# Kernel tuning notes

Measured on AMD Instinct MI355X. Metric: run time of the kernel, lower is better.

The kernel has to match this reference:

```python
import jax, jax.numpy as jnp
import numpy as np

D_MODEL = 1024
NUM_HEADS = 16
D_K = D_MODEL // NUM_HEADS
THETA = 10000.0
BATCH, SEQ = 2, 2048


def apply_rope(x, token_positions, theta):
    # x: [..., heads, seq, d_k]; interleaved pair rotation
    d = x.shape[-1]
    inv_freq = theta ** (-jnp.arange(0, d, 2, dtype=jnp.float32) / d)  # [d/2]
    ang = token_positions.astype(jnp.float32)[:, None] * inv_freq[None, :]  # [seq, d/2]
    cos, sin = jnp.cos(ang), jnp.sin(ang)  # broadcast over batch/heads
    x_even = x[..., 0::2]
    x_odd = x[..., 1::2]
    out_even = x_even * cos - x_odd * sin
    out_odd = x_even * sin + x_odd * cos
    out = jnp.stack([out_even, out_odd], axis=-1)  # [..., seq, d/2, 2]
    return out.reshape(x.shape)


def setup_inputs() -> dict:
    key = jax.random.key(0)
    ks = jax.random.split(key, 5)
    scale = 1.0 / np.sqrt(D_MODEL)
    return {
        "x": jax.random.normal(ks[0], (BATCH, SEQ, D_MODEL), dtype=jnp.float32),
        "wq": jax.random.normal(ks[1], (D_MODEL, D_MODEL), dtype=jnp.float32) * scale,
        "wk": jax.random.normal(ks[2], (D_MODEL, D_MODEL), dtype=jnp.float32) * scale,
        "wv": jax.random.normal(ks[3], (D_MODEL, D_MODEL), dtype=jnp.float32) * scale,
        "wo": jax.random.normal(ks[4], (D_MODEL, D_MODEL), dtype=jnp.float32) * scale,
        "token_positions": jnp.arange(SEQ, dtype=jnp.int32),
    }


def reference(x, wq, wk, wv, wo, token_positions):
    B, S, _ = x.shape
    # fused-style QKV projections: weight layout is [d_out, d_in]
    xq = jnp.einsum("bsd,kd->bsk", x, wq)
    xk = jnp.einsum("bsd,kd->bsk", x, wk)
    xv = jnp.einsum("bsd,vd->bsv", x, wv)
    # split heads: [b, h, s, d_h]
    def split(t):
        return t.reshape(B, S, NUM_HEADS, D_K).transpose(0, 2, 1, 3)
    xq, xk, xv = split(xq), split(xk), split(xv)
    xq = apply_rope(xq, token_positions, THETA)
    xk = apply_rope(xk, token_positions, THETA)
    scores = jnp.einsum("bhqd,bhkd->bhqk", xq, xk) / jnp.sqrt(jnp.float32(D_K))
    causal = jnp.tril(jnp.ones((S, S), dtype=bool))
    scores = jnp.where(causal, scores, -jnp.inf)
    attn = jax.nn.softmax(scores, axis=-1)
    out = jnp.einsum("bhqk,bhkd->bhqd", attn, xv)
    out = out.transpose(0, 2, 1, 3).reshape(B, S, D_MODEL)  # merge heads
    return jnp.einsum("bsv,dv->bsd", out, wo)
```

## Files before the change

### kernel.cpp

```cpp
#include <hip/hip_runtime.h>

typedef __attribute__((ext_vector_type(8))) short short8;
typedef __attribute__((ext_vector_type(4))) short short4v;
typedef __attribute__((ext_vector_type(4))) float floatx4;

__device__ inline float b2f(ushort u) {
    union { uint i; float f; } c; c.i = ((uint)u) << 16; return c.f;
}
__device__ inline ushort f2b(float f) {
    union { uint i; float f; } c; c.f = f;
    uint i = c.i;
    uint r = (i + 0x7FFFu + ((i >> 16) & 1u)) >> 16;
    return (ushort)r;
}
__device__ inline ushort f2b_fast(float f) {
    union { uint i; float f; } c; c.f = f;
    return (ushort)((c.i + 0x8000u) >> 16);
}

__device__ __forceinline__ void load_lds16(const ushort* g, ushort* l) {
    __builtin_amdgcn_global_load_lds((const __attribute__((address_space(1))) void*)g,
                                     (__attribute__((address_space(3))) void*)l, 16, 0, 0);
}

__global__ __launch_bounds__(256) void rope_tab_k(const int* __restrict__ pos,
                                                  float2* __restrict__ tab) {
    const int idx = blockIdx.x * 256 + threadIdx.x;
    const int s = idx >> 5, fi = idx & 31;
    const float inv = exp2f(-(float)fi * 0.41524101186092557f);
    const float ang = (float)pos[s] * inv;
    float sn, cs;
    sincosf(ang, &sn, &cs);
    tab[idx] = make_float2(cs, sn);
}

__global__ __launch_bounds__(256) void cvt4_k(const float* __restrict__ x,
                                              const float* __restrict__ wq,
                                              const float* __restrict__ wk,
                                              const float* __restrict__ wv,
                                              ushort* __restrict__ xb,
                                              ushort* __restrict__ wqb,
                                              ushort* __restrict__ wkb,
                                              ushort* __restrict__ wvb) {
    const int blk = blockIdx.x;
    const float* in; ushort* out; int base;
    if (blk < 2048)      { in = x;  out = xb;  base = blk; }
    else if (blk < 2560) { in = wq; out = wqb; base = blk - 2048; }
    else if (blk < 3072) { in = wk; out = wkb; base = blk - 2560; }
    else                 { in = wv; out = wvb; base = blk - 3072; }
    const int i = (base * 256 + threadIdx.x) * 8;
    float4 f0 = *(const float4*)(in + i);
    float4 f1 = *(const float4*)(in + i + 4);
    ushort u[8] = {f2b(f0.x), f2b(f0.y), f2b(f0.z), f2b(f0.w),
                   f2b(f1.x), f2b(f1.y), f2b(f1.z), f2b(f1.w)};
    *(uint4*)(out + i) = *(const uint4*)u;
}

__global__ __launch_bounds__(256) void cvt_k(const float* __restrict__ in,
                                             ushort* __restrict__ out, int n) {
    const int i = (blockIdx.x * 256 + threadIdx.x) * 8;
    if (i >= n) return;
    float4 f0 = *(const float4*)(in + i);
    float4 f1 = *(const float4*)(in + i + 4);
    ushort u[8] = {f2b(f0.x), f2b(f0.y), f2b(f0.z), f2b(f0.w),
                   f2b(f1.x), f2b(f1.y), f2b(f1.z), f2b(f1.w)};
    *(uint4*)(out + i) = *(const uint4*)u;
}

template <bool OUTF32>
__device__ __forceinline__ void gemm_body(ushort* As, ushort* Bs,
                                          const ushort* __restrict__ A,
                                          const ushort* __restrict__ B,
                                          void* __restrict__ C,
                                          int N, int m0, int n0,
                                          bool doRope, const float2* __restrict__ tab) {
    const int tid = threadIdx.x;
    const int wave = tid >> 6, lane = tid & 63;
    const int quad = lane >> 4, l16 = lane & 15;
    const int wm = (wave >> 1) * 64, wn = (wave & 1) * 64;

    floatx4 acc[4][4] = {};

    const int cA = tid, cB = tid + 256;
    const int rA = cA >> 2, jgA = ((cA & 3) - (rA >> 1)) & 3;
    const int rB = cB >> 2, jgB = ((cB & 3) - (rB >> 1)) & 3;
    const ushort* gaA = A + (size_t)(m0 + rA) * 1024 + jgA * 8;
    const ushort* gaB = A + (size_t)(m0 + rB) * 1024 + jgB * 8;
    const ushort* gbA = B + (size_t)(n0 + rA) * 1024 + jgA * 8;
    const ushort* gbB = B + (size_t)(n0 + rB) * 1024 + jgB * 8;

    load_lds16(gaA, As + cA * 8);
    load_lds16(gaB, As + cB * 8);
    load_lds16(gbA, Bs + cA * 8);
    load_lds16(gbB, Bs + cB * 8);
    __syncthreads();

    for (int kt = 0; kt < 32; ++kt) {
        const int cur = kt & 1;
        if (kt + 1 < 32) {
            const int nb = (cur ^ 1) * 4096;
            load_lds16(gaA + (kt + 1) * 32, As + nb + cA * 8);
            load_lds16(gaB + (kt + 1) * 32, As + nb + cB * 8);
            load_lds16(gbA + (kt + 1) * 32, Bs + nb + cA * 8);
            load_lds16(gbB + (kt + 1) * 32, Bs + nb + cB * 8);
        }
        const ushort* as = As + cur * 4096;
        const ushort* bs = Bs + cur * 4096;
        short8 af[4], bf[4];
#pragma unroll
        for (int i = 0; i < 4; ++i) {
            const int ra = wm + i * 16 + l16;
            const int rb = wn + i * 16 + l16;
            af[i] = *(const short8*)(as + ra * 32 + (((quad + (ra >> 1)) & 3) << 3));
            bf[i] = *(const short8*)(bs + rb * 32 + (((quad + (rb >> 1)) & 3) << 3));
        }
#pragma unroll
        for (int mi = 0; mi < 4; ++mi)
#pragma unroll
            for (int ni = 0; ni < 4; ++ni)
                acc[mi][ni] = __builtin_amdgcn_mfma_f32_16x16x32_bf16(af[mi], bf[ni], acc[mi][ni], 0, 0, 0);
        __syncthreads();
    }
#pragma unroll
    for (int mi = 0; mi < 4; ++mi) {
        const int row = m0 + wm + mi * 16 + quad * 4;
#pragma unroll
        for (int ni = 0; ni < 4; ++ni) {
            const int col = n0 + wn + ni * 16 + l16;
            const int fi = ((wn + ni * 16 + l16) & 63) >> 1;
#pragma unroll
            for (int r = 0; r < 4; ++r) {
                float v = acc[mi][ni][r];
                if (doRope) {
                    const float other = __shfl_xor(v, 1);
                    const float2 cs = tab[((row + r) & 2047) * 32 + fi];
                    v = (col & 1) ? (other * cs.y + v * cs.x) : (v * cs.x - other * cs.y);
                }
                if (OUTF32) ((float*)C)[(size_t)(row + r) * N + col] = v;
                else        ((ushort*)C)[(size_t)(row + r) * N + col] = f2b(v);
            }
        }
    }
}

__global__ __launch_bounds__(256) void gemm_qkv(const ushort* __restrict__ xb,
                                                const ushort* __restrict__ wqb,
                                                const ushort* __restrict__ wkb,
                                                const ushort* __restrict__ wvb,
                                                ushort* __restrict__ q,
                                                ushort* __restrict__ k,
                                                ushort* __restrict__ vt,
                                                const float2* __restrict__ tab) {
    __shared__ __align__(16) ushort As[8192], Bs[8192];
    const int blk = blockIdx.x;
    const int job = blk >> 8, r = blk & 255;
    const ushort *A, *B;
    ushort* C;
    int N, m0, n0;
    bool rope;
    if (job == 0)      { A = xb;  B = wqb; C = q;  N = 1024; m0 = (r >> 3) * 128; n0 = (r & 7) * 128; rope = true; }
    else if (job == 1) { A = xb;  B = wkb; C = k;  N = 1024; m0 = (r >> 3) * 128; n0 = (r & 7) * 128; rope = true; }
    else               { A = wvb; B = xb;  C = vt; N = 4096; m0 = (r & 7) * 128;  n0 = (r >> 3) * 128; rope = false; }
    gemm_body<false>(As, Bs, A, B, C, N, m0, n0, rope, tab);
}

__global__ __launch_bounds__(256) void gemm_o(const ushort* __restrict__ A,
                                              const ushort* __restrict__ B,
                                              float* __restrict__ C) {
    __shared__ __align__(16) ushort As[8192], Bs[8192];
    gemm_body<true>(As, Bs, A, B, C, 1024, blockIdx.y * 128, blockIdx.x * 128, false, nullptr);
}

__global__ __launch_bounds__(256) void attn_k(const ushort* __restrict__ Qg,
                                              const ushort* __restrict__ Kg,
                                              const ushort* __restrict__ Vtg,
                                              ushort* __restrict__ Og) {
    __shared__ __align__(16) ushort Ks[2][4096];
    __shared__ __align__(16) ushort Vs[2][4096];

    const int tid = threadIdx.x;
    const int wave = tid >> 6, lane = tid & 63;
    const int quad = lane >> 4, l16 = lane & 15;
    const int blk = blockIdx.x;
    const int bh = blk & 31, pr = blk >> 5;
    const int b = bh >> 4, h = bh & 15;
    const int bq = b * 2048;
    const int wl = wave * 16 + l16;

    const int cA = tid, cB = tid + 256;
    const int sA = cA >> 3, jA = ((cA & 7) - sA) & 7;
    const int sB = cB >> 3, jB = ((cB & 7) - sB) & 7;
    const ushort* kgA = Kg + (size_t)(bq + sA) * 1024 + h * 64 + jA * 8;
    const ushort* kgB = Kg + (size_t)(bq + sB) * 1024 + h * 64 + jB * 8;
    const ushort* vgA = Vtg + (size_t)(h * 64 + sA) * 4096 + bq + jA * 8;
    const ushort* vgB = Vtg + (size_t)(h * 64 + sB) * 4096 + bq + jB * 8;

    const float SCL = 0.18033688011112042f;

    for (int half = 0; half < 2; ++half) {
        const int qt = half ? (31 - pr) : pr;
        const int nk = qt + 1;
        const int dt = nk - 1;

        const ushort* qrow = Qg + (size_t)(bq + qt * 64 + wl) * 1024 + h * 64 + quad * 8;
        const short8 qf0 = *(const short8*)qrow;
        const short8 qf1 = *(const short8*)(qrow + 32);

        floatx4 od[4] = {};
        float l_st = 0.0f;

        load_lds16(kgA, &Ks[0][cA * 8]);
        load_lds16(kgB, &Ks[0][cB * 8]);
        load_lds16(vgA, &Vs[0][cA * 8]);
        load_lds16(vgB, &Vs[0][cB * 8]);
        __syncthreads();

        for (int kt = 0; kt < nk; ++kt) {
            const int cur = kt & 1;
            if (kt + 1 < nk) {
                const int nxt = cur ^ 1;
                load_lds16(kgA + (size_t)(kt + 1) * 65536, &Ks[nxt][cA * 8]);
                load_lds16(kgB + (size_t)(kt + 1) * 65536, &Ks[nxt][cB * 8]);
                load_lds16(vgA + (kt + 1) * 64, &Vs[nxt][cA * 8]);
                load_lds16(vgB + (kt + 1) * 64, &Vs[nxt][cB * 8]);
            }
            const ushort* kb = Ks[cur];
            const ushort* vb = Vs[cur];

            floatx4 st[4];
#pragma unroll
            for (int cb = 0; cb < 4; ++cb) {
                const int s = cb * 16 + l16;
                const int ch0 = s * 8 + ((quad + s) & 7);
                const int ch1 = s * 8 + ((quad + 4 + s) & 7);
                short8 kf0 = *(const short8*)(kb + ch0 * 8);
                short8 kf1 = *(const short8*)(kb + ch1 * 8);
                floatx4 z = {};
                z = __builtin_amdgcn_mfma_f32_16x16x32_bf16(kf0, qf0, z, 0, 0, 0);
                z = __builtin_amdgcn_mfma_f32_16x16x32_bf16(kf1, qf1, z, 0, 0, 0);
                st[cb] = z;
            }

            const bool diag = (kt == dt);
            float pv[4][4];
            float sum = 0.0f;
#pragma unroll
            for (int cb = 0; cb < 4; ++cb) {
                const int scb = cb * 16 + quad * 4;
#pragma unroll
                for (int r = 0; r < 4; ++r) {
                    float e = exp2f(st[cb][r] * SCL);
                    if (diag && (scb + r > wl)) e = 0.0f;
                    pv[cb][r] = e;
                    sum += e;
                }
            }
            sum += __shfl_xor(sum, 16);
            sum += __shfl_xor(sum, 32);
            l_st += sum;

            short4v pb[4];
#pragma unroll
            for (int cb = 0; cb < 4; ++cb) {
                short4v pk;
#pragma unroll
                for (int r = 0; r < 4; ++r) pk[r] = (short)f2b_fast(pv[cb][r]);
                pb[cb] = pk;
            }
#pragma unroll
            for (int db = 0; db < 4; ++db) {
                const int d = db * 16 + l16;
#pragma unroll
                for (int cb = 0; cb < 4; ++cb) {
                    const int j = cb * 2 + (quad >> 1);
                    const int ch = d * 8 + ((j + d) & 7);
                    short4v vf = *(const short4v*)(vb + ch * 8 + (quad & 1) * 4);
                    od[db] = __builtin_amdgcn_mfma_f32_16x16x16bf16_1k(vf, pb[cb], od[db], 0, 0, 0);
                }
            }
            __syncthreads();
        }

        const float linv = 1.0f / l_st;
        ushort* orow = Og + (size_t)(bq + qt * 64 + wl) * 1024 + h * 64 + quad * 4;
#pragma unroll
        for (int db = 0; db < 4; ++db) {
            uint2 w;
            w.x = (uint)f2b(od[db][0] * linv) | ((uint)f2b(od[db][1] * linv) << 16);
            w.y = (uint)f2b(od[db][2] * linv) | ((uint)f2b(od[db][3] * linv) << 16);
            *(uint2*)(orow + db * 16) = w;
        }
    }
}

extern "C" void kernel_launch(void* const* d_in, const int* in_sizes, int n_in,
                              void* d_out, int out_size, void* d_ws, size_t ws_size,
                              hipStream_t stream) {
    const float* x  = (const float*)d_in[0];
    const float* wq = (const float*)d_in[1];
    const float* wk = (const float*)d_in[2];
    const float* wv = (const float*)d_in[3];
    const float* wo = (const float*)d_in[4];
    const int* pos  = (const int*)d_in[5];

    const size_t NX = (size_t)4096 * 1024;
    const size_t NW = (size_t)1024 * 1024;

    ushort* q_ws  = (ushort*)d_ws;
    ushort* k_ws  = q_ws + NX;
    ushort* vt_ws = k_ws + NX;
    ushort* o_ws  = vt_ws + NX;
    ushort* xb  = (ushort*)d_out;
    ushort* wqb = xb + NX;
    ushort* wkb = wqb + NW;
    ushort* wvb = wkb + NW;
    float2* tab = (float2*)(wvb + NW);

    rope_tab_k<<<dim3(256), 256, 0, stream>>>(pos, tab);
    cvt4_k<<<dim3(3584), 256, 0, stream>>>(x, wq, wk, wv, xb, wqb, wkb, wvb);
    gemm_qkv<<<dim3(768), 256, 0, stream>>>(xb, wqb, wkb, wvb, q_ws, k_ws, vt_ws, tab);
    attn_k<<<dim3(512), 256, 0, stream>>>(q_ws, k_ws, vt_ws, o_ws);
    cvt_k<<<dim3(512), 256, 0, stream>>>(wo, q_ws, (int)NW);
    gemm_o<<<dim3(8, 32), 256, 0, stream>>>(o_ws, q_ws, (float*)d_out);
}
```

Before: 205.7 us.

## Split attention per query tile, fold rope table and softmax scale upstream

Attention now launches one block per query tile, ordered heaviest first, instead of pairing two tiles per block. It also adds an occupancy hint, wave priority around the MFMA sections, hoisted LDS offsets and packed bf16 conversion. The rope sin/cos table is computed inside the conversion kernel to remove a launch, and the softmax scale is applied to Q in the QKV GEMM epilogue. Scaling Q before the bf16 rounding slightly changes numerics, and more blocks add per-block setup overhead.

```diff
diff --git a/kernel.cpp b/kernel.cpp
--- a/kernel.cpp
+++ b/kernel.cpp
@@ -4,34 +4,16 @@
 typedef __attribute__((ext_vector_type(4))) short short4v;
 typedef __attribute__((ext_vector_type(4))) float floatx4;
 
-__device__ inline float b2f(ushort u) {
-    union { uint i; float f; } c; c.i = ((uint)u) << 16; return c.f;
-}
 __device__ inline ushort f2b(float f) {
     union { uint i; float f; } c; c.f = f;
     uint i = c.i;
     uint r = (i + 0x7FFFu + ((i >> 16) & 1u)) >> 16;
     return (ushort)r;
 }
-__device__ inline ushort f2b_fast(float f) {
-    union { uint i; float f; } c; c.f = f;
-    return (ushort)((c.i + 0x8000u) >> 16);
-}
 
 __device__ __forceinline__ void load_lds16(const ushort* g, ushort* l) {
     __builtin_amdgcn_global_load_lds((const __attribute__((address_space(1))) void*)g,
                                      (__attribute__((address_space(3))) void*)l, 16, 0, 0);
-}
-
-__global__ __launch_bounds__(256) void rope_tab_k(const int* __restrict__ pos,
-                                                  float2* __restrict__ tab) {
-    const int idx = blockIdx.x * 256 + threadIdx.x;
-    const int s = idx >> 5, fi = idx & 31;
-    const float inv = exp2f(-(float)fi * 0.41524101186092557f);
-    const float ang = (float)pos[s] * inv;
-    float sn, cs;
-    sincosf(ang, &sn, &cs);
-    tab[idx] = make_float2(cs, sn);
 }
 
 __global__ __launch_bounds__(256) void cvt4_k(const float* __restrict__ x,
@@ -41,8 +23,20 @@
                                               ushort* __restrict__ xb,
                                               ushort* __restrict__ wqb,
                                               ushort* __restrict__ wkb,
-                                              ushort* __restrict__ wvb) {
+                                              ushort* __restrict__ wvb,
+                                              const int* __restrict__ pos,
+                                              float2* __restrict__ tab) {
     const int blk = blockIdx.x;
+    if (blk >= 3584) {
+        const int idx = (blk - 3584) * 256 + threadIdx.x;
+        const int s = idx >> 5, fi = idx & 31;
+        const float inv = exp2f(-(float)fi * 0.41524101186092557f);
+        const float ang = (float)pos[s] * inv;
+        float sn, cs;
+        sincosf(ang, &sn, &cs);
+        tab[idx] = make_float2(cs, sn);
+        return;
+    }
     const float* in; ushort* out; int base;
     if (blk < 2048)      { in = x;  out = xb;  base = blk; }
     else if (blk < 2560) { in = wq; out = wqb; base = blk - 2048; }
@@ -73,7 +67,8 @@
                                           const ushort* __restrict__ B,
                                           void* __restrict__ C,
                                           int N, int m0, int n0,
-                                          bool doRope, const float2* __restrict__ tab) {
+                                          bool doRope, const float2* __restrict__ tab,
+                                          float oscale) {
     const int tid = threadIdx.x;
     const int wave = tid >> 6, lane = tid & 63;
     const int quad = lane >> 4, l16 = lane & 15;
@@ -136,6 +131,7 @@
                     const float2 cs = tab[((row + r) & 2047) * 32 + fi];
                     v = (col & 1) ? (other * cs.y + v * cs.x) : (v * cs.x - other * cs.y);
                 }
+                v *= oscale;
                 if (OUTF32) ((float*)C)[(size_t)(row + r) * N + col] = v;
                 else        ((ushort*)C)[(size_t)(row + r) * N + col] = f2b(v);
             }
@@ -158,23 +154,24 @@
     ushort* C;
     int N, m0, n0;
     bool rope;
-    if (job == 0)      { A = xb;  B = wqb; C = q;  N = 1024; m0 = (r >> 3) * 128; n0 = (r & 7) * 128; rope = true; }
-    else if (job == 1) { A = xb;  B = wkb; C = k;  N = 1024; m0 = (r >> 3) * 128; n0 = (r & 7) * 128; rope = true; }
-    else               { A = wvb; B = xb;  C = vt; N = 4096; m0 = (r & 7) * 128;  n0 = (r >> 3) * 128; rope = false; }
-    gemm_body<false>(As, Bs, A, B, C, N, m0, n0, rope, tab);
+    float osc;
+    if (job == 0)      { A = xb;  B = wqb; C = q;  N = 1024; m0 = (r >> 3) * 128; n0 = (r & 7) * 128; rope = true;  osc = 0.18033688011112042f; }
+    else if (job == 1) { A = xb;  B = wkb; C = k;  N = 1024; m0 = (r >> 3) * 128; n0 = (r & 7) * 128; rope = true;  osc = 1.0f; }
+    else               { A = wvb; B = xb;  C = vt; N = 4096; m0 = (r & 7) * 128;  n0 = (r >> 3) * 128; rope = false; osc = 1.0f; }
+    gemm_body<false>(As, Bs, A, B, C, N, m0, n0, rope, tab, osc);
 }
 
 __global__ __launch_bounds__(256) void gemm_o(const ushort* __restrict__ A,
                                               const ushort* __restrict__ B,
                                               float* __restrict__ C) {
     __shared__ __align__(16) ushort As[8192], Bs[8192];
-    gemm_body<true>(As, Bs, A, B, C, 1024, blockIdx.y * 128, blockIdx.x * 128, false, nullptr);
-}
-
-__global__ __launch_bounds__(256) void attn_k(const ushort* __restrict__ Qg,
-                                              const ushort* __restrict__ Kg,
-                                              const ushort* __restrict__ Vtg,
-                                              ushort* __restrict__ Og) {
+    gemm_body<true>(As, Bs, A, B, C, 1024, blockIdx.y * 128, blockIdx.x * 128, false, nullptr, 1.0f);
+}
+
+__global__ __launch_bounds__(256, 4) void attn_k(const ushort* __restrict__ Qg,
+                                                 const ushort* __restrict__ Kg,
+                                                 const ushort* __restrict__ Vtg,
+                                                 ushort* __restrict__ Og) {
     __shared__ __align__(16) ushort Ks[2][4096];
     __shared__ __align__(16) ushort Vs[2][4096];
 
@@ -182,10 +179,12 @@
     const int wave = tid >> 6, lane = tid & 63;
     const int quad = lane >> 4, l16 = lane & 15;
     const int blk = blockIdx.x;
-    const int bh = blk & 31, pr = blk >> 5;
+    const int bh = blk & 31;
+    const int qt = 31 - (blk >> 5);
     const int b = bh >> 4, h = bh & 15;
     const int bq = b * 2048;
     const int wl = wave * 16 + l16;
+    const int nk = qt + 1, dt = nk - 1;
 
     const int cA = tid, cB = tid + 256;
     const int sA = cA >> 3, jA = ((cA & 7) - sA) & 7;
@@ -195,101 +194,107 @@
     const ushort* vgA = Vtg + (size_t)(h * 64 + sA) * 4096 + bq + jA * 8;
     const ushort* vgB = Vtg + (size_t)(h * 64 + sB) * 4096 + bq + jB * 8;
 
-    const float SCL = 0.18033688011112042f;
-
-    for (int half = 0; half < 2; ++half) {
-        const int qt = half ? (31 - pr) : pr;
-        const int nk = qt + 1;
-        const int dt = nk - 1;
-
-        const ushort* qrow = Qg + (size_t)(bq + qt * 64 + wl) * 1024 + h * 64 + quad * 8;
-        const short8 qf0 = *(const short8*)qrow;
-        const short8 qf1 = *(const short8*)(qrow + 32);
-
-        floatx4 od[4] = {};
-        float l_st = 0.0f;
-
-        load_lds16(kgA, &Ks[0][cA * 8]);
-        load_lds16(kgB, &Ks[0][cB * 8]);
-        load_lds16(vgA, &Vs[0][cA * 8]);
-        load_lds16(vgB, &Vs[0][cB * 8]);
+    const int kb0 = l16 * 64 + (((quad + l16) & 7) << 3);
+    const int kb1 = l16 * 64 + (((quad + 4 + l16) & 7) << 3);
+    int vbs[4];
+#pragma unroll
+    for (int cb = 0; cb < 4; ++cb)
+        vbs[cb] = l16 * 64 + (((cb * 2 + (quad >> 1) + l16) & 7) << 3) + (quad & 1) * 4;
+
+    const ushort* qrow = Qg + (size_t)(bq + qt * 64 + wl) * 1024 + h * 64 + quad * 8;
+    const short8 qf0 = *(const short8*)qrow;
+    const short8 qf1 = *(const short8*)(qrow + 32);
+
+    floatx4 od[4] = {};
+    float l_st = 0.0f;
+
+    load_lds16(kgA, &Ks[0][cA * 8]);
+    load_lds16(kgB, &Ks[0][cB * 8]);
+    load_lds16(vgA, &Vs[0][cA * 8]);
+    load_lds16(vgB, &Vs[0][cB * 8]);
+    __syncthreads();
+
+    const ushort* kgA2 = kgA + 65536;
+    const ushort* kgB2 = kgB + 65536;
+    const ushort* vgA2 = vgA + 64;
+    const ushort* vgB2 = vgB + 64;
+
+    for (int kt = 0; kt < nk; ++kt) {
+        const int cur = kt & 1;
+        if (kt + 1 < nk) {
+            const int nxt = cur ^ 1;
+            load_lds16(kgA2, &Ks[nxt][cA * 8]);
+            load_lds16(kgB2, &Ks[nxt][cB * 8]);
+            load_lds16(vgA2, &Vs[nxt][cA * 8]);
+            load_lds16(vgB2, &Vs[nxt][cB * 8]);
+            kgA2 += 65536; kgB2 += 65536; vgA2 += 64; vgB2 += 64;
+        }
+        const ushort* kc = &Ks[cur][0];
+        const ushort* vc = &Vs[cur][0];
+
+        floatx4 st[4];
+        __builtin_amdgcn_s_setprio(1);
+#pragma unroll
+        for (int cb = 0; cb < 4; ++cb) {
+            short8 kf0 = *(const short8*)(kc + kb0 + cb * 1024);
+            short8 kf1 = *(const short8*)(kc + kb1 + cb * 1024);
+            floatx4 z = {};
+            z = __builtin_amdgcn_mfma_f32_16x16x32_bf16(kf0, qf0, z, 0, 0, 0);
+            z = __builtin_amdgcn_mfma_f32_16x16x32_bf16(kf1, qf1, z, 0, 0, 0);
+            st[cb] = z;
+        }
+        __builtin_amdgcn_s_setprio(0);
+
+        const bool diag = (kt == dt);
+        float pv[4][4];
+        float sum = 0.0f;
+#pragma unroll
+        for (int cb = 0; cb < 4; ++cb) {
+            const int scb = cb * 16 + quad * 4;
+#pragma unroll
+            for (int r = 0; r < 4; ++r) {
+                float e = exp2f(st[cb][r]);
+                if (diag && (scb + r > wl)) e = 0.0f;
+                pv[cb][r] = e;
+                sum += e;
+            }
+        }
+        sum += __shfl_xor(sum, 16);
+        sum += __shfl_xor(sum, 32);
+        l_st += sum;
+
+        short4v pb[4];
+#pragma unroll
+        for (int cb = 0; cb < 4; ++cb) {
+            uint lo_, hi_;
+            asm("v_cvt_pk_bf16_f32 %0, %1, %2" : "=v"(lo_) : "v"(pv[cb][0]), "v"(pv[cb][1]));
+            asm("v_cvt_pk_bf16_f32 %0, %1, %2" : "=v"(hi_) : "v"(pv[cb][2]), "v"(pv[cb][3]));
+            union { uint u[2]; short4v s; } cvu;
+            cvu.u[0] = lo_; cvu.u[1] = hi_;
+            pb[cb] = cvu.s;
+        }
+
+        __builtin_amdgcn_s_setprio(1);
+#pragma unroll
+        for (int db = 0; db < 4; ++db) {
+#pragma unroll
+            for (int cb = 0; cb < 4; ++cb) {
+                short4v vf = *(const short4v*)(vc + vbs[cb] + db * 1024);
+                od[db] = __builtin_amdgcn_mfma_f32_16x16x16bf16_1k(vf, pb[cb], od[db], 0, 0, 0);
+            }
+        }
+        __builtin_amdgcn_s_setprio(0);
         __syncthreads();
-
-        for (int kt = 0; kt < nk; ++kt) {
-            const int cur = kt & 1;
-            if (kt + 1 < nk) {
-                const int nxt = cur ^ 1;
-                load_lds16(kgA + (size_t)(kt + 1) * 65536, &Ks[nxt][cA * 8]);
-                load_lds16(kgB + (size_t)(kt + 1) * 65536, &Ks[nxt][cB * 8]);
-                load_lds16(vgA + (kt + 1) * 64, &Vs[nxt][cA * 8]);
-                load_lds16(vgB + (kt + 1) * 64, &Vs[nxt][cB * 8]);
-            }
-            const ushort* kb = Ks[cur];
-            const ushort* vb = Vs[cur];
-
-            floatx4 st[4];
-#pragma unroll
-            for (int cb = 0; cb < 4; ++cb) {
-                const int s = cb * 16 + l16;
-                const int ch0 = s * 8 + ((quad + s) & 7);
-                const int ch1 = s * 8 + ((quad + 4 + s) & 7);
-                short8 kf0 = *(const short8*)(kb + ch0 * 8);
-                short8 kf1 = *(const short8*)(kb + ch1 * 8);
-                floatx4 z = {};
-                z = __builtin_amdgcn_mfma_f32_16x16x32_bf16(kf0, qf0, z, 0, 0, 0);
-                z = __builtin_amdgcn_mfma_f32_16x16x32_bf16(kf1, qf1, z, 0, 0, 0);
-                st[cb] = z;
-            }
-
-            const bool diag = (kt == dt);
-            float pv[4][4];
-            float sum = 0.0f;
-#pragma unroll
-            for (int cb = 0; cb < 4; ++cb) {
-                const int scb = cb * 16 + quad * 4;
-#pragma unroll
-                for (int r = 0; r < 4; ++r) {
-                    float e = exp2f(st[cb][r] * SCL);
-                    if (diag && (scb + r > wl)) e = 0.0f;
-                    pv[cb][r] = e;
-                    sum += e;
-                }
-            }
-            sum += __shfl_xor(sum, 16);
-            sum += __shfl_xor(sum, 32);
-            l_st += sum;
-
-            short4v pb[4];
-#pragma unroll
-            for (int cb = 0; cb < 4; ++cb) {
-                short4v pk;
-#pragma unroll
-                for (int r = 0; r < 4; ++r) pk[r] = (short)f2b_fast(pv[cb][r]);
-                pb[cb] = pk;
-            }
-#pragma unroll
-            for (int db = 0; db < 4; ++db) {
-                const int d = db * 16 + l16;
-#pragma unroll
-                for (int cb = 0; cb < 4; ++cb) {
-                    const int j = cb * 2 + (quad >> 1);
-                    const int ch = d * 8 + ((j + d) & 7);
-                    short4v vf = *(const short4v*)(vb + ch * 8 + (quad & 1) * 4);
-                    od[db] = __builtin_amdgcn_mfma_f32_16x16x16bf16_1k(vf, pb[cb], od[db], 0, 0, 0);
-                }
-            }
-            __syncthreads();
-        }
-
-        const float linv = 1.0f / l_st;
-        ushort* orow = Og + (size_t)(bq + qt * 64 + wl) * 1024 + h * 64 + quad * 4;
-#pragma unroll
-        for (int db = 0; db < 4; ++db) {
-            uint2 w;
-            w.x = (uint)f2b(od[db][0] * linv) | ((uint)f2b(od[db][1] * linv) << 16);
-            w.y = (uint)f2b(od[db][2] * linv) | ((uint)f2b(od[db][3] * linv) << 16);
-            *(uint2*)(orow + db * 16) = w;
-        }
+    }
+
+    const float linv = 1.0f / l_st;
+    ushort* orow = Og + (size_t)(bq + qt * 64 + wl) * 1024 + h * 64 + quad * 4;
+#pragma unroll
+    for (int db = 0; db < 4; ++db) {
+        uint2 w;
+        w.x = (uint)f2b(od[db][0] * linv) | ((uint)f2b(od[db][1] * linv) << 16);
+        w.y = (uint)f2b(od[db][2] * linv) | ((uint)f2b(od[db][3] * linv) << 16);
+        *(uint2*)(orow + db * 16) = w;
     }
 }
 
@@ -316,10 +321,9 @@
     ushort* wvb = wkb + NW;
     float2* tab = (float2*)(wvb + NW);
 
-    rope_tab_k<<<dim3(256), 256, 0, stream>>>(pos, tab);
-    cvt4_k<<<dim3(3584), 256, 0, stream>>>(x, wq, wk, wv, xb, wqb, wkb, wvb);
+    cvt4_k<<<dim3(3840), 256, 0, stream>>>(x, wq, wk, wv, xb, wqb, wkb, wvb, pos, tab);
     gemm_qkv<<<dim3(768), 256, 0, stream>>>(xb, wqb, wkb, wvb, q_ws, k_ws, vt_ws, tab);
-    attn_k<<<dim3(512), 256, 0, stream>>>(q_ws, k_ws, vt_ws, o_ws);
+    attn_k<<<dim3(1024), 256, 0, stream>>>(q_ws, k_ws, vt_ws, o_ws);
     cvt_k<<<dim3(512), 256, 0, stream>>>(wo, q_ws, (int)NW);
     gemm_o<<<dim3(8, 32), 256, 0, stream>>>(o_ws, q_ws, (float*)d_out);
 }
```

Result: faster. 201.2 us (-2.2%).
